# Kernel tuning notes

Hardware: AMD Instinct MI355X
Metric: run time of the kernel (lower is better)

## Reference

```python
import jax, jax.numpy as jnp
import numpy as np

SCORE_THRESHOLD = 0.5
IOU_THRESHOLD = 0.5


def _pairwise_iou(boxes):
    # boxes: [N, 4] in xyxy
    x1, y1, x2, y2 = boxes[:, 0], boxes[:, 1], boxes[:, 2], boxes[:, 3]
    area = (x2 - x1) * (y2 - y1)  # [N]
    ix1 = jnp.maximum(x1[:, None], x1[None, :])
    iy1 = jnp.maximum(y1[:, None], y1[None, :])
    ix2 = jnp.minimum(x2[:, None], x2[None, :])
    iy2 = jnp.minimum(y2[:, None], y2[None, :])
    iw = jnp.clip(ix2 - ix1, 0.0)
    ih = jnp.clip(iy2 - iy1, 0.0)
    inter = iw * ih  # [N, N]
    union = area[:, None] + area[None, :] - inter
    return inter / jnp.maximum(union, 1e-9)


def setup_inputs() -> dict:
    key = jax.random.key(0)
    rtdetr_raw_out = jax.random.uniform(key, (1, 8192, 5), dtype=jnp.float32)
    return {"rtdetr_raw_out": rtdetr_raw_out}


def reference(rtdetr_raw_out):
    x = rtdetr_raw_out[0]                      # [N, 5]
    cxcywh = x[:, :4]
    conf = x[:, 4]
    conf = conf / jnp.max(conf)                # normalize by max score
    cx, cy, w, h = cxcywh[:, 0], cxcywh[:, 1], cxcywh[:, 2], cxcywh[:, 3]
    xyxy = jnp.stack([cx - w * 0.5, cy - h * 0.5, cx + w * 0.5, cy + h * 0.5], axis=1)
    valid = conf >= SCORE_THRESHOLD            # score filter
    N = xyxy.shape[0]
    # sort by descending score (torchvision nms processes boxes in score order)
    order = jnp.argsort(-conf)
    boxes_s = xyxy[order]
    scores_s = conf[order]
    valid_s = valid[order]
    iou = _pairwise_iou(boxes_s)               # [N, N]
    idx = jnp.arange(N)

    def body(i, keep):
        # if box i survives, suppress all lower-score boxes with IoU > thr
        sup = keep[i] & (iou[i] > IOU_THRESHOLD) & (idx > i)
        return keep & ~sup

    keep = jax.lax.fori_loop(0, N, body, valid_s)
    out = jnp.concatenate([boxes_s, scores_s[:, None]], axis=1)  # [N, 5]
    # fixed-shape output: suppressed / below-threshold rows are zeroed
    return jnp.where(keep[:, None], out, 0.0)
```

## Files before the change

kernel.cpp:

```cpp
#include <hip/hip_runtime.h>
#include <cstdint>

typedef unsigned long long ull;

#define N_BOX 8192
#define N_WORDS 128
#define CH 512
#define WPC 8
#define NCH 16

#define OFF_TB     0
#define OFF_TD     3932160
#define OFF_BOXES  4456448
#define OFF_SCORES 4587520
#define OFF_RANK   4620288
#define OFF_MASK   4653056
#define OFF_MAXC   4654080
#define OFF_VB     4654084

__device__ __forceinline__ int rows_before(int c) {
    return 8192 * c - 256 * c * (c + 1);
}

__device__ __forceinline__ ull make_key(float s, int idx) {
    return (((ull)__float_as_uint(s)) << 13) | (ull)(8191 - idx);
}

__device__ __forceinline__ float box_area(float4 b) {
    return __fmul_rn(__fsub_rn(b.z, b.x), __fsub_rn(b.w, b.y));
}

__device__ __forceinline__ bool iou_gt_half(float4 a, float aarea, float4 b, float barea) {
    float ix1 = fmaxf(a.x, b.x);
    float iy1 = fmaxf(a.y, b.y);
    float ix2 = fminf(a.z, b.z);
    float iy2 = fminf(a.w, b.w);
    float iw = fmaxf(__fsub_rn(ix2, ix1), 0.0f);
    float ih = fmaxf(__fsub_rn(iy2, iy1), 0.0f);
    float inter = __fmul_rn(iw, ih);
    float uni = __fsub_rn(__fadd_rn(aarea, barea), inter);
    float iou = __fdiv_rn(inter, fmaxf(uni, 1e-9f));
    return iou > 0.5f;
}

__global__ __launch_bounds__(1024) void k1_max_zero(const float* __restrict__ in,
                                                    float* __restrict__ maxc,
                                                    int* __restrict__ rank,
                                                    ull* __restrict__ mask,
                                                    int* __restrict__ vbp) {
    int t = threadIdx.x;
    float m = 0.0f;
    for (int k = t; k < N_BOX; k += 1024) m = fmaxf(m, in[k * 5 + 4]);
    for (int off = 32; off; off >>= 1) m = fmaxf(m, __shfl_down(m, off));
    __shared__ float wm[16];
    if ((t & 63) == 0) wm[t >> 6] = m;
    __syncthreads();
    if (t == 0) {
        float mm = wm[0];
        for (int k = 1; k < 16; ++k) mm = fmaxf(mm, wm[k]);
        *maxc = mm;
        *vbp = 0;
    }
    for (int k = t; k < N_BOX; k += 1024) rank[k] = 0;
    if (t < N_WORDS) mask[t] = 0ull;
}

__global__ __launch_bounds__(256) void k2_rank(const float* __restrict__ in,
                                               const float* __restrict__ maxc_p,
                                               int* __restrict__ rank) {
    __shared__ ull keys[1024];
    int t = threadIdx.x;
    int bx = blockIdx.x;
    int it = bx & 31;
    int jt = bx >> 5;
    float maxc = *maxc_p;
    for (int r = 0; r < 4; ++r) {
        int j = jt * 1024 + r * 256 + t;
        float s = __fdiv_rn(in[j * 5 + 4], maxc);
        keys[r * 256 + t] = make_key(s, j);
    }
    __syncthreads();
    int i = it * 256 + t;
    ull ki = make_key(__fdiv_rn(in[i * 5 + 4], maxc), i);
    int cnt = 0;
    #pragma unroll 8
    for (int k = 0; k < 1024; ++k) cnt += (keys[k] > ki) ? 1 : 0;
    atomicAdd(&rank[i], cnt);
}

__global__ __launch_bounds__(256) void k3_scatter(const float* __restrict__ in,
                                                  const int* __restrict__ rank,
                                                  const float* __restrict__ maxc_p,
                                                  float4* __restrict__ boxes4,
                                                  float* __restrict__ scores,
                                                  ull* __restrict__ mask,
                                                  int* __restrict__ vbp) {
    int i = blockIdx.x * 256 + threadIdx.x;
    float cx = in[i * 5 + 0];
    float cy = in[i * 5 + 1];
    float w  = in[i * 5 + 2];
    float h  = in[i * 5 + 3];
    float c  = in[i * 5 + 4];
    float maxc = *maxc_p;
    float s = __fdiv_rn(c, maxc);
    int r = rank[i];
    float4 b;
    b.x = __fsub_rn(cx, __fmul_rn(w, 0.5f));
    b.y = __fsub_rn(cy, __fmul_rn(h, 0.5f));
    b.z = __fadd_rn(cx, __fmul_rn(w, 0.5f));
    b.w = __fadd_rn(cy, __fmul_rn(h, 0.5f));
    boxes4[r] = b;
    scores[r] = s;
    if (s >= 0.5f) {
        atomicOr(&mask[r >> 6], 1ull << (r & 63));
        atomicAdd(vbp, 1);
    }
}

__global__ __launch_bounds__(256) void k4_build(const float4* __restrict__ boxes4,
                                                const float* __restrict__ scores,
                                                ull* __restrict__ TB,
                                                ull* __restrict__ TD) {
    __shared__ float4 sb[CH];
    __shared__ float sa[CH];
    int bid = blockIdx.x;
    int t = threadIdx.x;
    int c, j0;
    bool diag;
    if (bid >= 1920) {
        diag = true;
        int d = bid - 1920;
        c = d >> 4;
        j0 = (d & 15) * 32;
    } else {
        diag = false;
        c = 0;
        int rem = bid;
        while (rem >= 240 - 16 * c) { rem -= 240 - 16 * c; ++c; }
        j0 = CH * (c + 1) + rem * 32;
    }
    if (scores[c * CH] < 0.5f) return;
    if (!diag && scores[j0] < 0.5f) return;

    for (int i = t; i < CH; i += 256) {
        float4 b = boxes4[c * CH + i];
        sb[i] = b;
        sa[i] = box_area(b);
    }
    __syncthreads();

    int w = t & 7;
    int jj = j0 + (t >> 3);
    if (diag) {
        int jl = jj;
        float4 me = sb[jl];
        float ma = sa[jl];
        int wj = jl >> 6;
        int lim = (w < wj) ? 64 : ((w == wj) ? (jl & 63) : 0);
        ull bits = 0;
        for (int k = 0; k < lim; ++k)
            if (iou_gt_half(sb[w * 64 + k], sa[w * 64 + k], me, ma)) bits |= 1ull << k;
        TD[c * 4096 + w * 512 + jl] = bits;
    } else {
        int j = jj;
        float4 me = boxes4[j];
        float ma = box_area(me);
        ull bits = 0;
        for (int k = 0; k < 64; ++k)
            if (iou_gt_half(sb[w * 64 + k], sa[w * 64 + k], me, ma)) bits |= 1ull << k;
        TB[(size_t)(rows_before(c) + (j - CH * (c + 1))) * WPC + w] = bits;
    }
}

__global__ __launch_bounds__(1024) void k5_nms(const float4* __restrict__ boxes4,
                                               const float* __restrict__ scores,
                                               const ull* __restrict__ gmask,
                                               const ull* __restrict__ TBg,
                                               const ull* __restrict__ TDg,
                                               const int* __restrict__ vbp,
                                               float* __restrict__ out) {
    __shared__ ull TDb[2][CH * WPC];
    __shared__ unsigned amask32[2 * N_WORDS];
    __shared__ ull keptw[WPC];
    __shared__ int svb;
    int t = threadIdx.x;
    int lane = t & 63;
    int wave = t >> 6;

    if (t < 2 * N_WORDS) amask32[t] = ((const unsigned*)gmask)[t];
    if (t == 0) svb = *vbp;
    if (t < WPC) keptw[t] = 0;
    for (int i = t; i < CH * WPC; i += 1024) TDb[0][i] = TDg[i];
    __syncthreads();

    int vb = svb;
    int nchv = (vb + CH - 1) / CH;
    int cur = 0;
    for (int c = 0; c < nchv; ++c) {
        if (wave == 0) {
            const ull* T = TDb[cur];
            ull alive[WPC];
            #pragma unroll
            for (int w = 0; w < WPC; ++w)
                alive[w] = (ull)amask32[c * 16 + 2 * w] |
                           ((ull)amask32[c * 16 + 2 * w + 1] << 32);
            #pragma unroll
            for (int w = 0; w < WPC; ++w) {
                ull word = alive[w];
                if (!word) continue;
                ull td = T[w * 512 + w * 64 + lane];
                ull a2 = word, kept = 0;
                while (a2 & ~kept) {
                    bool al = (a2 >> lane) & 1;
                    bool kp = (kept >> lane) & 1;
                    ull nk = __ballot(al && !kp && ((td & a2) == 0));
                    ull nd = __ballot(al && !kp && ((td & kept) != 0));
                    kept |= nk;
                    a2 &= ~nd;
                }
                alive[w] = kept;
                #pragma unroll
                for (int j = 0; j < WPC; ++j) {
                    if (j <= w) continue;
                    if (!alive[j]) continue;
                    ull m = T[w * 512 + j * 64 + lane];
                    alive[j] &= ~__ballot((m & kept) != 0);
                }
            }
            if (lane == 0) {
                #pragma unroll
                for (int w = 0; w < WPC; ++w) {
                    amask32[c * 16 + 2 * w]     = (unsigned)alive[w];
                    amask32[c * 16 + 2 * w + 1] = (unsigned)(alive[w] >> 32);
                    keptw[w] = alive[w];
                }
            }
        } else if (c + 1 < nchv) {
            int base = (c + 1) * CH * WPC;
            for (int i = t - 64; i < CH * WPC; i += 960) TDb[cur ^ 1][i] = TDg[base + i];
        }
        __syncthreads();

        ull kw[WPC];
        ull anyk = 0;
        #pragma unroll
        for (int k = 0; k < WPC; ++k) { kw[k] = keptw[k]; anyk |= kw[k]; }
        if (anyk) {
            const ull* TBc = TBg + (size_t)rows_before(c) * WPC;
            int jbase = CH * (c + 1);
            for (int j = jbase + t; j < vb; j += 1024) {
                if ((amask32[j >> 5] >> (j & 31)) & 1u) {
                    const ull* r = TBc + (size_t)(j - jbase) * WPC;
                    ull acc = 0;
                    #pragma unroll
                    for (int k = 0; k < WPC; ++k) acc |= r[k] & kw[k];
                    if (acc) atomicAnd(&amask32[j >> 5], ~(1u << (j & 31)));
                }
            }
        }
        cur ^= 1;
        __syncthreads();
    }

    #pragma unroll
    for (int rr = 0; rr < 8; ++rr) {
        int j = t * 8 + rr;
        bool kept = (amask32[j >> 5] >> (j & 31)) & 1u;
        float4 b = boxes4[j];
        float s = scores[j];
        out[j * 5 + 0] = kept ? b.x : 0.0f;
        out[j * 5 + 1] = kept ? b.y : 0.0f;
        out[j * 5 + 2] = kept ? b.z : 0.0f;
        out[j * 5 + 3] = kept ? b.w : 0.0f;
        out[j * 5 + 4] = kept ? s   : 0.0f;
    }
}

extern "C" void kernel_launch(void* const* d_in, const int* in_sizes, int n_in,
                              void* d_out, int out_size, void* d_ws, size_t ws_size,
                              hipStream_t stream) {
    const float* in = (const float*)d_in[0];
    char* ws = (char*)d_ws;
    ull* TB        = (ull*)(ws + OFF_TB);
    ull* TD        = (ull*)(ws + OFF_TD);
    float4* boxes4 = (float4*)(ws + OFF_BOXES);
    float* scores  = (float*)(ws + OFF_SCORES);
    int* rank      = (int*)(ws + OFF_RANK);
    ull* mask      = (ull*)(ws + OFF_MASK);
    float* maxc    = (float*)(ws + OFF_MAXC);
    int* vbp       = (int*)(ws + OFF_VB);
    float* out     = (float*)d_out;

    k1_max_zero<<<1, 1024, 0, stream>>>(in, maxc, rank, mask, vbp);
    k2_rank<<<256, 256, 0, stream>>>(in, maxc, rank);
    k3_scatter<<<32, 256, 0, stream>>>(in, rank, maxc, boxes4, scores, mask, vbp);
    k4_build<<<2176, 256, 0, stream>>>(boxes4, scores, TB, TD);
    k5_nms<<<1, 1024, 0, stream>>>(boxes4, scores, mask, TB, TD, vbp, out);
}
```

Before: 144.7 us.

## Fuse all NMS stages into one cooperative kernel with grid syncs

Replaces the five separate kernel launches (max, rank, scatter, IoU bitmask build, serial NMS) with a single cooperative kernel of 256 blocks of 1024 threads, separated by grid-wide barriers. The ranking now loads all 8192 keys into shared memory per block and does the counting within a block instead of using global atomics. The bitmask build is remapped onto 544 virtual tiles of 128 rows. This aims to remove per-launch overhead and the global rank zeroing. In exchange it pays for grid syncs, needs cooperative launch residency, and uses a 64KB shared union that may lower occupancy.

```diff
diff --git a/kernel.cpp b/kernel.cpp
--- a/kernel.cpp
+++ b/kernel.cpp
@@ -1,21 +1,22 @@
 #include <hip/hip_runtime.h>
+#include <hip/hip_cooperative_groups.h>
 #include <cstdint>
 
+namespace cg = cooperative_groups;
 typedef unsigned long long ull;
 
 #define N_BOX 8192
 #define N_WORDS 128
 #define CH 512
 #define WPC 8
-#define NCH 16
+#define NBLK 256
 
 #define OFF_TB     0
 #define OFF_TD     3932160
 #define OFF_BOXES  4456448
 #define OFF_SCORES 4587520
-#define OFF_RANK   4620288
+#define OFF_PART   4620288
 #define OFF_MASK   4653056
-#define OFF_MAXC   4654080
 #define OFF_VB     4654084
 
 __device__ __forceinline__ int rows_before(int c) {
@@ -43,154 +44,144 @@
     return iou > 0.5f;
 }
 
-__global__ __launch_bounds__(1024) void k1_max_zero(const float* __restrict__ in,
-                                                    float* __restrict__ maxc,
-                                                    int* __restrict__ rank,
-                                                    ull* __restrict__ mask,
-                                                    int* __restrict__ vbp) {
-    int t = threadIdx.x;
-    float m = 0.0f;
-    for (int k = t; k < N_BOX; k += 1024) m = fmaxf(m, in[k * 5 + 4]);
-    for (int off = 32; off; off >>= 1) m = fmaxf(m, __shfl_down(m, off));
-    __shared__ float wm[16];
-    if ((t & 63) == 0) wm[t >> 6] = m;
-    __syncthreads();
-    if (t == 0) {
-        float mm = wm[0];
-        for (int k = 1; k < 16; ++k) mm = fmaxf(mm, wm[k]);
-        *maxc = mm;
-        *vbp = 0;
-    }
-    for (int k = t; k < N_BOX; k += 1024) rank[k] = 0;
-    if (t < N_WORDS) mask[t] = 0ull;
-}
-
-__global__ __launch_bounds__(256) void k2_rank(const float* __restrict__ in,
-                                               const float* __restrict__ maxc_p,
-                                               int* __restrict__ rank) {
-    __shared__ ull keys[1024];
-    int t = threadIdx.x;
-    int bx = blockIdx.x;
-    int it = bx & 31;
-    int jt = bx >> 5;
-    float maxc = *maxc_p;
-    for (int r = 0; r < 4; ++r) {
-        int j = jt * 1024 + r * 256 + t;
-        float s = __fdiv_rn(in[j * 5 + 4], maxc);
-        keys[r * 256 + t] = make_key(s, j);
-    }
-    __syncthreads();
-    int i = it * 256 + t;
-    ull ki = make_key(__fdiv_rn(in[i * 5 + 4], maxc), i);
-    int cnt = 0;
-    #pragma unroll 8
-    for (int k = 0; k < 1024; ++k) cnt += (keys[k] > ki) ? 1 : 0;
-    atomicAdd(&rank[i], cnt);
-}
-
-__global__ __launch_bounds__(256) void k3_scatter(const float* __restrict__ in,
-                                                  const int* __restrict__ rank,
-                                                  const float* __restrict__ maxc_p,
-                                                  float4* __restrict__ boxes4,
-                                                  float* __restrict__ scores,
-                                                  ull* __restrict__ mask,
-                                                  int* __restrict__ vbp) {
-    int i = blockIdx.x * 256 + threadIdx.x;
-    float cx = in[i * 5 + 0];
-    float cy = in[i * 5 + 1];
-    float w  = in[i * 5 + 2];
-    float h  = in[i * 5 + 3];
-    float c  = in[i * 5 + 4];
-    float maxc = *maxc_p;
-    float s = __fdiv_rn(c, maxc);
-    int r = rank[i];
-    float4 b;
-    b.x = __fsub_rn(cx, __fmul_rn(w, 0.5f));
-    b.y = __fsub_rn(cy, __fmul_rn(h, 0.5f));
-    b.z = __fadd_rn(cx, __fmul_rn(w, 0.5f));
-    b.w = __fadd_rn(cy, __fmul_rn(h, 0.5f));
-    boxes4[r] = b;
-    scores[r] = s;
-    if (s >= 0.5f) {
-        atomicOr(&mask[r >> 6], 1ull << (r & 63));
-        atomicAdd(vbp, 1);
-    }
-}
-
-__global__ __launch_bounds__(256) void k4_build(const float4* __restrict__ boxes4,
-                                                const float* __restrict__ scores,
-                                                ull* __restrict__ TB,
-                                                ull* __restrict__ TD) {
-    __shared__ float4 sb[CH];
-    __shared__ float sa[CH];
-    int bid = blockIdx.x;
-    int t = threadIdx.x;
-    int c, j0;
-    bool diag;
-    if (bid >= 1920) {
-        diag = true;
-        int d = bid - 1920;
-        c = d >> 4;
-        j0 = (d & 15) * 32;
-    } else {
-        diag = false;
-        c = 0;
-        int rem = bid;
-        while (rem >= 240 - 16 * c) { rem -= 240 - 16 * c; ++c; }
-        j0 = CH * (c + 1) + rem * 32;
-    }
-    if (scores[c * CH] < 0.5f) return;
-    if (!diag && scores[j0] < 0.5f) return;
-
-    for (int i = t; i < CH; i += 256) {
-        float4 b = boxes4[c * CH + i];
-        sb[i] = b;
-        sa[i] = box_area(b);
-    }
-    __syncthreads();
-
-    int w = t & 7;
-    int jj = j0 + (t >> 3);
-    if (diag) {
-        int jl = jj;
-        float4 me = sb[jl];
-        float ma = sa[jl];
-        int wj = jl >> 6;
-        int lim = (w < wj) ? 64 : ((w == wj) ? (jl & 63) : 0);
-        ull bits = 0;
-        for (int k = 0; k < lim; ++k)
-            if (iou_gt_half(sb[w * 64 + k], sa[w * 64 + k], me, ma)) bits |= 1ull << k;
-        TD[c * 4096 + w * 512 + jl] = bits;
-    } else {
-        int j = jj;
-        float4 me = boxes4[j];
-        float ma = box_area(me);
-        ull bits = 0;
-        for (int k = 0; k < 64; ++k)
-            if (iou_gt_half(sb[w * 64 + k], sa[w * 64 + k], me, ma)) bits |= 1ull << k;
-        TB[(size_t)(rows_before(c) + (j - CH * (c + 1))) * WPC + w] = bits;
-    }
-}
-
-__global__ __launch_bounds__(1024) void k5_nms(const float4* __restrict__ boxes4,
-                                               const float* __restrict__ scores,
-                                               const ull* __restrict__ gmask,
-                                               const ull* __restrict__ TBg,
-                                               const ull* __restrict__ TDg,
-                                               const int* __restrict__ vbp,
-                                               float* __restrict__ out) {
-    __shared__ ull TDb[2][CH * WPC];
+struct SMemB { ull keys[N_BOX]; };
+struct SMemD { float4 sb[CH]; float sa[CH]; };
+struct SMemE { ull TDb[2][CH * WPC]; };
+union SMemU { SMemB b; SMemD d; SMemE e; };
+
+__global__ __launch_bounds__(1024, 4) void fused_nms(
+        const float* __restrict__ in,
+        ull* __restrict__ TB, ull* __restrict__ TD,
+        float4* __restrict__ boxes4, float* __restrict__ scores,
+        float* __restrict__ partials, ull* __restrict__ maskg,
+        int* __restrict__ vbp, float* __restrict__ out)
+{
+    __shared__ SMemU sm;
     __shared__ unsigned amask32[2 * N_WORDS];
     __shared__ ull keptw[WPC];
+    __shared__ float smax;
+    __shared__ int rnk[32];
     __shared__ int svb;
+    cg::grid_group grid = cg::this_grid();
+    int bid = blockIdx.x;
     int t = threadIdx.x;
     int lane = t & 63;
     int wave = t >> 6;
 
-    if (t < 2 * N_WORDS) amask32[t] = ((const unsigned*)gmask)[t];
+    if (t < 32) {
+        float c = in[(bid * 32 + t) * 5 + 4];
+        for (int off = 16; off; off >>= 1) c = fmaxf(c, __shfl_down(c, off));
+        if (t == 0) partials[bid] = c;
+    }
+    if (bid == 0) {
+        if (t < N_WORDS) maskg[t] = 0ull;
+        if (t == 0) *vbp = 0;
+    }
+    grid.sync();
+
+    if (t < 64) {
+        float m = fmaxf(fmaxf(partials[t], partials[t + 64]),
+                        fmaxf(partials[t + 128], partials[t + 192]));
+        for (int off = 32; off; off >>= 1) m = fmaxf(m, __shfl_down(m, off));
+        if (t == 0) smax = m;
+    }
+    if (t < 32) rnk[t] = 0;
+    __syncthreads();
+    float maxc = smax;
+    #pragma unroll
+    for (int r = 0; r < 8; ++r) {
+        int j = r * 1024 + t;
+        sm.b.keys[j] = make_key(__fdiv_rn(in[j * 5 + 4], maxc), j);
+    }
+    __syncthreads();
+    {
+        int i = bid * 32 + (t & 31);
+        ull ki = sm.b.keys[i];
+        int slice = t >> 5;
+        int cnt = 0;
+        #pragma unroll 8
+        for (int k = 0; k < 256; ++k) cnt += (sm.b.keys[slice * 256 + k] > ki) ? 1 : 0;
+        atomicAdd(&rnk[t & 31], cnt);
+    }
+    __syncthreads();
+
+    if (t < 32) {
+        int ii = bid * 32 + t;
+        float cx = in[ii * 5 + 0];
+        float cy = in[ii * 5 + 1];
+        float w  = in[ii * 5 + 2];
+        float h  = in[ii * 5 + 3];
+        float s  = __fdiv_rn(in[ii * 5 + 4], maxc);
+        int r = rnk[t];
+        float4 b;
+        b.x = __fsub_rn(cx, __fmul_rn(w, 0.5f));
+        b.y = __fsub_rn(cy, __fmul_rn(h, 0.5f));
+        b.z = __fadd_rn(cx, __fmul_rn(w, 0.5f));
+        b.w = __fadd_rn(cy, __fmul_rn(h, 0.5f));
+        boxes4[r] = b;
+        scores[r] = s;
+        if (s >= 0.5f) {
+            atomicOr(&maskg[r >> 6], 1ull << (r & 63));
+            atomicAdd(vbp, 1);
+        }
+    }
+    grid.sync();
+
+    for (int vt = bid; vt < 544; vt += NBLK) {
+        int c, jt;
+        bool diag;
+        if (vt < 64) { diag = true; c = vt >> 2; jt = vt & 3; }
+        else {
+            diag = false;
+            int id = vt - 64;
+            c = 0;
+            while (id >= 60 - 4 * c) { id -= 60 - 4 * c; ++c; }
+            jt = id;
+        }
+        bool active = (scores[c * CH] >= 0.5f);
+        int j0 = diag ? (jt * 128) : (CH * (c + 1) + jt * 128);
+        if (active && !diag) active = (scores[j0] >= 0.5f);
+        if (active) {
+            __syncthreads();
+            if (t < CH) {
+                float4 b = boxes4[c * CH + t];
+                sm.d.sb[t] = b;
+                sm.d.sa[t] = box_area(b);
+            }
+            __syncthreads();
+            int r = t >> 3;
+            int w = t & 7;
+            if (diag) {
+                int jl = j0 + r;
+                float4 me = sm.d.sb[jl];
+                float ma = sm.d.sa[jl];
+                int wj = jl >> 6;
+                int lim = (w < wj) ? 64 : ((w == wj) ? (jl & 63) : 0);
+                ull bits = 0;
+                for (int k = 0; k < lim; ++k)
+                    if (iou_gt_half(sm.d.sb[w * 64 + k], sm.d.sa[w * 64 + k], me, ma))
+                        bits |= 1ull << k;
+                TD[c * 4096 + w * 512 + jl] = bits;
+            } else {
+                int j = j0 + r;
+                float4 me = boxes4[j];
+                float ma = box_area(me);
+                ull bits = 0;
+                for (int k = 0; k < 64; ++k)
+                    if (iou_gt_half(sm.d.sb[w * 64 + k], sm.d.sa[w * 64 + k], me, ma))
+                        bits |= 1ull << k;
+                TB[(size_t)(rows_before(c) + (j - CH * (c + 1))) * WPC + w] = bits;
+            }
+        }
+    }
+    grid.sync();
+
+    if (bid != 0) return;
+
+    if (t < 2 * N_WORDS) amask32[t] = ((const unsigned*)maskg)[t];
     if (t == 0) svb = *vbp;
     if (t < WPC) keptw[t] = 0;
-    for (int i = t; i < CH * WPC; i += 1024) TDb[0][i] = TDg[i];
+    for (int i2 = t; i2 < CH * WPC; i2 += 1024) sm.e.TDb[0][i2] = TD[i2];
     __syncthreads();
 
     int vb = svb;
@@ -198,7 +189,7 @@
     int cur = 0;
     for (int c = 0; c < nchv; ++c) {
         if (wave == 0) {
-            const ull* T = TDb[cur];
+            const ull* T = sm.e.TDb[cur];
             ull alive[WPC];
             #pragma unroll
             for (int w = 0; w < WPC; ++w)
@@ -237,7 +228,8 @@
             }
         } else if (c + 1 < nchv) {
             int base = (c + 1) * CH * WPC;
-            for (int i = t - 64; i < CH * WPC; i += 960) TDb[cur ^ 1][i] = TDg[base + i];
+            for (int i2 = t - 64; i2 < CH * WPC; i2 += 960)
+                sm.e.TDb[cur ^ 1][i2] = TD[base + i2];
         }
         __syncthreads();
 
@@ -246,7 +238,7 @@
         #pragma unroll
         for (int k = 0; k < WPC; ++k) { kw[k] = keptw[k]; anyk |= kw[k]; }
         if (anyk) {
-            const ull* TBc = TBg + (size_t)rows_before(c) * WPC;
+            const ull* TBc = TB + (size_t)rows_before(c) * WPC;
             int jbase = CH * (c + 1);
             for (int j = jbase + t; j < vb; j += 1024) {
                 if ((amask32[j >> 5] >> (j & 31)) & 1u) {
@@ -285,15 +277,14 @@
     ull* TD        = (ull*)(ws + OFF_TD);
     float4* boxes4 = (float4*)(ws + OFF_BOXES);
     float* scores  = (float*)(ws + OFF_SCORES);
-    int* rank      = (int*)(ws + OFF_RANK);
-    ull* mask      = (ull*)(ws + OFF_MASK);
-    float* maxc    = (float*)(ws + OFF_MAXC);
+    float* partials= (float*)(ws + OFF_PART);
+    ull* maskg     = (ull*)(ws + OFF_MASK);
     int* vbp       = (int*)(ws + OFF_VB);
     float* out     = (float*)d_out;
 
-    k1_max_zero<<<1, 1024, 0, stream>>>(in, maxc, rank, mask, vbp);
-    k2_rank<<<256, 256, 0, stream>>>(in, maxc, rank);
-    k3_scatter<<<32, 256, 0, stream>>>(in, rank, maxc, boxes4, scores, mask, vbp);
-    k4_build<<<2176, 256, 0, stream>>>(boxes4, scores, TB, TD);
-    k5_nms<<<1, 1024, 0, stream>>>(boxes4, scores, mask, TB, TD, vbp, out);
-}
+    void* args[] = { (void*)&in, (void*)&TB, (void*)&TD, (void*)&boxes4,
+                     (void*)&scores, (void*)&partials, (void*)&maskg,
+                     (void*)&vbp, (void*)&out };
+    hipLaunchCooperativeKernel(reinterpret_cast<void*>(fused_nms),
+                               dim3(NBLK), dim3(1024), args, 0, stream);
+}
```

Result: slower. 213.0 us (+47.3%).

## Replace column suppression scan with per-kept-box row bitmask and ballot-based ranking

Applied to the files above, without the earlier changes.

The cross-chunk suppression matrix is now stored row-major per box (`sup[i][W]`, 80 words wide), so each kept box clears alive bits through atomic ANDs on its own row. Before, every candidate scanned a column. The rank kernel counts with wave ballots and popcount instead of per-thread comparison loops over shared memory. The max reduction is split across 32 blocks using an integer atomicMax. `SUPW` caps suppression at 5120 boxes, which assumes the valid count stays under that limit. The atomicMax also relies on `maxc` not holding a larger stale value from a previous call.

```diff
diff --git a/kernel.cpp b/kernel.cpp
--- a/kernel.cpp
+++ b/kernel.cpp
@@ -7,20 +7,16 @@
 #define N_WORDS 128
 #define CH 512
 #define WPC 8
-#define NCH 16
-
-#define OFF_TB     0
-#define OFF_TD     3932160
-#define OFF_BOXES  4456448
-#define OFF_SCORES 4587520
-#define OFF_RANK   4620288
-#define OFF_MASK   4653056
-#define OFF_MAXC   4654080
-#define OFF_VB     4654084
-
-__device__ __forceinline__ int rows_before(int c) {
-    return 8192 * c - 256 * c * (c + 1);
-}
+#define SUPW 80
+
+#define OFF_SUP    0
+#define OFF_TD     5242880
+#define OFF_BOXES  5767168
+#define OFF_SCORES 5898240
+#define OFF_RANK   5931008
+#define OFF_MASK   5963776
+#define OFF_MAXC   5964800
+#define OFF_VB     5964804
 
 __device__ __forceinline__ ull make_key(float s, int idx) {
     return (((ull)__float_as_uint(s)) << 13) | (ull)(8191 - idx);
@@ -43,49 +39,52 @@
     return iou > 0.5f;
 }
 
-__global__ __launch_bounds__(1024) void k1_max_zero(const float* __restrict__ in,
-                                                    float* __restrict__ maxc,
-                                                    int* __restrict__ rank,
-                                                    ull* __restrict__ mask,
-                                                    int* __restrict__ vbp) {
+__global__ __launch_bounds__(256) void k1_max_zero(const float* __restrict__ in,
+                                                   int* __restrict__ maxci,
+                                                   int* __restrict__ rank,
+                                                   ull* __restrict__ mask,
+                                                   int* __restrict__ vbp) {
     int t = threadIdx.x;
-    float m = 0.0f;
-    for (int k = t; k < N_BOX; k += 1024) m = fmaxf(m, in[k * 5 + 4]);
-    for (int off = 32; off; off >>= 1) m = fmaxf(m, __shfl_down(m, off));
-    __shared__ float wm[16];
-    if ((t & 63) == 0) wm[t >> 6] = m;
+    int i = blockIdx.x * 256 + t;
+    float c = in[i * 5 + 4];
+    for (int off = 32; off; off >>= 1) c = fmaxf(c, __shfl_down(c, off));
+    __shared__ float wm[4];
+    if ((t & 63) == 0) wm[t >> 6] = c;
     __syncthreads();
     if (t == 0) {
-        float mm = wm[0];
-        for (int k = 1; k < 16; ++k) mm = fmaxf(mm, wm[k]);
-        *maxc = mm;
-        *vbp = 0;
-    }
-    for (int k = t; k < N_BOX; k += 1024) rank[k] = 0;
-    if (t < N_WORDS) mask[t] = 0ull;
-}
-
-__global__ __launch_bounds__(256) void k2_rank(const float* __restrict__ in,
-                                               const float* __restrict__ maxc_p,
-                                               int* __restrict__ rank) {
-    __shared__ ull keys[1024];
+        float m = fmaxf(fmaxf(wm[0], wm[1]), fmaxf(wm[2], wm[3]));
+        atomicMax(maxci, __float_as_int(m));
+    }
+    rank[i] = 0;
+    if (blockIdx.x == 0) {
+        if (t < N_WORDS) mask[t] = 0ull;
+        if (t == 0) *vbp = 0;
+    }
+}
+
+__global__ __launch_bounds__(1024) void k2_rank(const float* __restrict__ in,
+                                                const float* __restrict__ maxc_p,
+                                                int* __restrict__ rank) {
     int t = threadIdx.x;
-    int bx = blockIdx.x;
-    int it = bx & 31;
-    int jt = bx >> 5;
+    int lane = t & 63;
+    int g = blockIdx.x * 16 + (t >> 6);
+    int jg = g & 127;
+    int ibase = (g >> 7) * 256;
     float maxc = *maxc_p;
-    for (int r = 0; r < 4; ++r) {
-        int j = jt * 1024 + r * 256 + t;
-        float s = __fdiv_rn(in[j * 5 + 4], maxc);
-        keys[r * 256 + t] = make_key(s, j);
-    }
-    __syncthreads();
-    int i = it * 256 + t;
-    ull ki = make_key(__fdiv_rn(in[i * 5 + 4], maxc), i);
-    int cnt = 0;
-    #pragma unroll 8
-    for (int k = 0; k < 1024; ++k) cnt += (keys[k] > ki) ? 1 : 0;
-    atomicAdd(&rank[i], cnt);
+    int j = jg * 64 + lane;
+    ull kj = make_key(__fdiv_rn(in[j * 5 + 4], maxc), j);
+    #pragma unroll 1
+    for (int blk = 0; blk < 4; ++blk) {
+        int cnt = 0;
+        #pragma unroll 8
+        for (int ii = 0; ii < 64; ++ii) {
+            int i = ibase + blk * 64 + ii;
+            ull ki = make_key(__fdiv_rn(in[i * 5 + 4], maxc), i);
+            int pc = __popcll(__ballot(kj > ki));
+            cnt = (lane == ii) ? pc : cnt;
+        }
+        atomicAdd(&rank[ibase + blk * 64 + lane], cnt);
+    }
 }
 
 __global__ __launch_bounds__(256) void k3_scatter(const float* __restrict__ in,
@@ -119,63 +118,70 @@
 
 __global__ __launch_bounds__(256) void k4_build(const float4* __restrict__ boxes4,
                                                 const float* __restrict__ scores,
-                                                ull* __restrict__ TB,
+                                                ull* __restrict__ sup,
                                                 ull* __restrict__ TD) {
-    __shared__ float4 sb[CH];
-    __shared__ float sa[CH];
     int bid = blockIdx.x;
     int t = threadIdx.x;
-    int c, j0;
-    bool diag;
-    if (bid >= 1920) {
-        diag = true;
-        int d = bid - 1920;
-        c = d >> 4;
-        j0 = (d & 15) * 32;
+    if (bid < 4096) {
+        int it = bid >> 5;
+        int wt = bid & 31;
+        int i0 = it * 64;
+        if (wt * 4 >= SUPW) return;
+        if ((wt + 1) * 256 <= i0) return;
+        if (scores[i0] < 0.5f) return;
+        if (scores[wt * 256] < 0.5f) return;
+        __shared__ float4 bi[64];
+        __shared__ float4 bj[256];
+        if (t < 64) bi[t] = boxes4[i0 + t];
+        bj[t] = boxes4[wt * 256 + t];
+        __syncthreads();
+        int il = t >> 2;
+        int wl = t & 3;
+        int i = i0 + il;
+        float4 a = bi[il];
+        float aarea = box_area(a);
+        ull word = 0ull;
+        #pragma unroll 4
+        for (int k = 0; k < 64; ++k) {
+            float4 b = bj[wl * 64 + k];
+            if (iou_gt_half(a, aarea, b, box_area(b))) word |= (1ull << k);
+        }
+        sup[(size_t)i * SUPW + wt * 4 + wl] = word;
     } else {
-        diag = false;
-        c = 0;
-        int rem = bid;
-        while (rem >= 240 - 16 * c) { rem -= 240 - 16 * c; ++c; }
-        j0 = CH * (c + 1) + rem * 32;
-    }
-    if (scores[c * CH] < 0.5f) return;
-    if (!diag && scores[j0] < 0.5f) return;
-
-    for (int i = t; i < CH; i += 256) {
-        float4 b = boxes4[c * CH + i];
-        sb[i] = b;
-        sa[i] = box_area(b);
-    }
-    __syncthreads();
-
-    int w = t & 7;
-    int jj = j0 + (t >> 3);
-    if (diag) {
-        int jl = jj;
+        int d = bid - 4096;
+        int c = d >> 3;
+        int jt = d & 7;
+        if (scores[c * CH] < 0.5f) return;
+        __shared__ float4 sb[CH];
+        __shared__ float sa[CH];
+        for (int i2 = t; i2 < CH; i2 += 256) {
+            float4 b = boxes4[c * CH + i2];
+            sb[i2] = b;
+            sa[i2] = box_area(b);
+        }
+        __syncthreads();
+        int r = t >> 2;
+        int wl = t & 3;
+        int jl = jt * 64 + r;
         float4 me = sb[jl];
         float ma = sa[jl];
         int wj = jl >> 6;
-        int lim = (w < wj) ? 64 : ((w == wj) ? (jl & 63) : 0);
-        ull bits = 0;
-        for (int k = 0; k < lim; ++k)
-            if (iou_gt_half(sb[w * 64 + k], sa[w * 64 + k], me, ma)) bits |= 1ull << k;
-        TD[c * 4096 + w * 512 + jl] = bits;
-    } else {
-        int j = jj;
-        float4 me = boxes4[j];
-        float ma = box_area(me);
-        ull bits = 0;
-        for (int k = 0; k < 64; ++k)
-            if (iou_gt_half(sb[w * 64 + k], sa[w * 64 + k], me, ma)) bits |= 1ull << k;
-        TB[(size_t)(rows_before(c) + (j - CH * (c + 1))) * WPC + w] = bits;
+        #pragma unroll
+        for (int p = 0; p < 2; ++p) {
+            int w = wl + p * 4;
+            int lim = (w < wj) ? 64 : ((w == wj) ? (jl & 63) : 0);
+            ull bits = 0;
+            for (int k = 0; k < lim; ++k)
+                if (iou_gt_half(sb[w * 64 + k], sa[w * 64 + k], me, ma)) bits |= 1ull << k;
+            TD[c * 4096 + w * 512 + jl] = bits;
+        }
     }
 }
 
 __global__ __launch_bounds__(1024) void k5_nms(const float4* __restrict__ boxes4,
                                                const float* __restrict__ scores,
                                                const ull* __restrict__ gmask,
-                                               const ull* __restrict__ TBg,
+                                               const ull* __restrict__ supg,
                                                const ull* __restrict__ TDg,
                                                const int* __restrict__ vbp,
                                                float* __restrict__ out) {
@@ -190,11 +196,13 @@
     if (t < 2 * N_WORDS) amask32[t] = ((const unsigned*)gmask)[t];
     if (t == 0) svb = *vbp;
     if (t < WPC) keptw[t] = 0;
-    for (int i = t; i < CH * WPC; i += 1024) TDb[0][i] = TDg[i];
+    for (int i2 = t; i2 < CH * WPC; i2 += 1024) TDb[0][i2] = TDg[i2];
     __syncthreads();
 
     int vb = svb;
     int nchv = (vb + CH - 1) / CH;
+    int wv = (vb + 63) >> 6;
+    int Wlim = (wv < SUPW) ? wv : SUPW;
     int cur = 0;
     for (int c = 0; c < nchv; ++c) {
         if (wave == 0) {
@@ -207,7 +215,7 @@
             #pragma unroll
             for (int w = 0; w < WPC; ++w) {
                 ull word = alive[w];
-                if (!word) continue;
+                if (!word) { if (lane == 0) keptw[w] = 0; continue; }
                 ull td = T[w * 512 + w * 64 + lane];
                 ull a2 = word, kept = 0;
                 while (a2 & ~kept) {
@@ -226,36 +234,44 @@
                     ull m = T[w * 512 + j * 64 + lane];
                     alive[j] &= ~__ballot((m & kept) != 0);
                 }
+                if (lane == 0) keptw[w] = kept;
             }
             if (lane == 0) {
                 #pragma unroll
                 for (int w = 0; w < WPC; ++w) {
                     amask32[c * 16 + 2 * w]     = (unsigned)alive[w];
                     amask32[c * 16 + 2 * w + 1] = (unsigned)(alive[w] >> 32);
-                    keptw[w] = alive[w];
                 }
             }
         } else if (c + 1 < nchv) {
             int base = (c + 1) * CH * WPC;
-            for (int i = t - 64; i < CH * WPC; i += 960) TDb[cur ^ 1][i] = TDg[base + i];
+            for (int i2 = t - 64; i2 < CH * WPC; i2 += 960)
+                TDb[cur ^ 1][i2] = TDg[base + i2];
         }
         __syncthreads();
 
-        ull kw[WPC];
-        ull anyk = 0;
-        #pragma unroll
-        for (int k = 0; k < WPC; ++k) { kw[k] = keptw[k]; anyk |= kw[k]; }
-        if (anyk) {
-            const ull* TBc = TBg + (size_t)rows_before(c) * WPC;
-            int jbase = CH * (c + 1);
-            for (int j = jbase + t; j < vb; j += 1024) {
-                if ((amask32[j >> 5] >> (j & 31)) & 1u) {
-                    const ull* r = TBc + (size_t)(j - jbase) * WPC;
-                    ull acc = 0;
-                    #pragma unroll
-                    for (int k = 0; k < WPC; ++k) acc |= r[k] & kw[k];
-                    if (acc) atomicAnd(&amask32[j >> 5], ~(1u << (j & 31)));
+        int kidx = 0;
+        for (int w8 = 0; w8 < WPC; ++w8) {
+            ull kw = keptw[w8];
+            while (kw) {
+                int b = __builtin_ctzll(kw);
+                kw &= kw - 1;
+                if ((kidx & 15) == wave) {
+                    int i = c * CH + w8 * 64 + b;
+                    const ull* row = supg + (size_t)i * SUPW;
+                    for (int Wb = WPC * (c + 1); Wb < Wlim; Wb += 64) {
+                        int W = Wb + lane;
+                        if (W < Wlim) {
+                            ull s = row[W];
+                            if (s) {
+                                unsigned lo = (unsigned)s, hi = (unsigned)(s >> 32);
+                                if (lo) atomicAnd(&amask32[2 * W], ~lo);
+                                if (hi) atomicAnd(&amask32[2 * W + 1], ~hi);
+                            }
+                        }
+                    }
                 }
+                ++kidx;
             }
         }
         cur ^= 1;
@@ -281,7 +297,7 @@
                               hipStream_t stream) {
     const float* in = (const float*)d_in[0];
     char* ws = (char*)d_ws;
-    ull* TB        = (ull*)(ws + OFF_TB);
+    ull* sup       = (ull*)(ws + OFF_SUP);
     ull* TD        = (ull*)(ws + OFF_TD);
     float4* boxes4 = (float4*)(ws + OFF_BOXES);
     float* scores  = (float*)(ws + OFF_SCORES);
@@ -291,9 +307,9 @@
     int* vbp       = (int*)(ws + OFF_VB);
     float* out     = (float*)d_out;
 
-    k1_max_zero<<<1, 1024, 0, stream>>>(in, maxc, rank, mask, vbp);
-    k2_rank<<<256, 256, 0, stream>>>(in, maxc, rank);
+    k1_max_zero<<<32, 256, 0, stream>>>(in, (int*)maxc, rank, mask, vbp);
+    k2_rank<<<256, 1024, 0, stream>>>(in, maxc, rank);
     k3_scatter<<<32, 256, 0, stream>>>(in, rank, maxc, boxes4, scores, mask, vbp);
-    k4_build<<<2176, 256, 0, stream>>>(boxes4, scores, TB, TD);
-    k5_nms<<<1, 1024, 0, stream>>>(boxes4, scores, mask, TB, TD, vbp, out);
-}
+    k4_build<<<4224, 256, 0, stream>>>(boxes4, scores, sup, TD);
+    k5_nms<<<1, 1024, 0, stream>>>(boxes4, scores, mask, sup, TD, vbp, out);
+}
```

New measurement: 274.9 us. +90.1%, slower.

## Fuse max, rank and scatter kernels; derive valid mask from sorted prefix count

Applied to the files above, without the earlier changes.

Merges the max-reduction, rank-counting and scatter kernels into one kernel. Each of 32 blocks recomputes the global max and builds all 8192 sort keys in shared memory, then counts ranks for its own 256 boxes. The NMS kernel now counts valid scores itself and builds the alive mask as a prefix, since sorted valid boxes are contiguous. This removes the per-row mask test in the suppression loop. The aim is to cut two kernel launches plus the global atomics and zeroing, at the cost of redundant max and key work in every block.

```diff
diff --git a/kernel.cpp b/kernel.cpp
--- a/kernel.cpp
+++ b/kernel.cpp
@@ -7,16 +7,11 @@
 #define N_WORDS 128
 #define CH 512
 #define WPC 8
-#define NCH 16
 
 #define OFF_TB     0
 #define OFF_TD     3932160
 #define OFF_BOXES  4456448
 #define OFF_SCORES 4587520
-#define OFF_RANK   4620288
-#define OFF_MASK   4653056
-#define OFF_MAXC   4654080
-#define OFF_VB     4654084
 
 __device__ __forceinline__ int rows_before(int c) {
     return 8192 * c - 256 * c * (c + 1);
@@ -43,81 +38,69 @@
     return iou > 0.5f;
 }
 
-__global__ __launch_bounds__(1024) void k1_max_zero(const float* __restrict__ in,
-                                                    float* __restrict__ maxc,
-                                                    int* __restrict__ rank,
-                                                    ull* __restrict__ mask,
-                                                    int* __restrict__ vbp) {
+__global__ __launch_bounds__(1024) void ka_rank_scatter(const float* __restrict__ in,
+                                                        float4* __restrict__ boxes4,
+                                                        float* __restrict__ scores) {
+    __shared__ ull skeys[N_BOX];
+    __shared__ float wm[16];
+    __shared__ int rnk[256];
     int t = threadIdx.x;
+    int bid = blockIdx.x;
+
+    float cf[8];
     float m = 0.0f;
-    for (int k = t; k < N_BOX; k += 1024) m = fmaxf(m, in[k * 5 + 4]);
+    #pragma unroll
+    for (int k = 0; k < 8; ++k) {
+        cf[k] = in[(k * 1024 + t) * 5 + 4];
+        m = fmaxf(m, cf[k]);
+    }
     for (int off = 32; off; off >>= 1) m = fmaxf(m, __shfl_down(m, off));
-    __shared__ float wm[16];
     if ((t & 63) == 0) wm[t >> 6] = m;
-    __syncthreads();
-    if (t == 0) {
-        float mm = wm[0];
-        for (int k = 1; k < 16; ++k) mm = fmaxf(mm, wm[k]);
-        *maxc = mm;
-        *vbp = 0;
-    }
-    for (int k = t; k < N_BOX; k += 1024) rank[k] = 0;
-    if (t < N_WORDS) mask[t] = 0ull;
-}
-
-__global__ __launch_bounds__(256) void k2_rank(const float* __restrict__ in,
-                                               const float* __restrict__ maxc_p,
-                                               int* __restrict__ rank) {
-    __shared__ ull keys[1024];
-    int t = threadIdx.x;
-    int bx = blockIdx.x;
-    int it = bx & 31;
-    int jt = bx >> 5;
-    float maxc = *maxc_p;
-    for (int r = 0; r < 4; ++r) {
-        int j = jt * 1024 + r * 256 + t;
-        float s = __fdiv_rn(in[j * 5 + 4], maxc);
-        keys[r * 256 + t] = make_key(s, j);
-    }
-    __syncthreads();
-    int i = it * 256 + t;
-    ull ki = make_key(__fdiv_rn(in[i * 5 + 4], maxc), i);
-    int cnt = 0;
-    #pragma unroll 8
-    for (int k = 0; k < 1024; ++k) cnt += (keys[k] > ki) ? 1 : 0;
-    atomicAdd(&rank[i], cnt);
-}
-
-__global__ __launch_bounds__(256) void k3_scatter(const float* __restrict__ in,
-                                                  const int* __restrict__ rank,
-                                                  const float* __restrict__ maxc_p,
-                                                  float4* __restrict__ boxes4,
-                                                  float* __restrict__ scores,
-                                                  ull* __restrict__ mask,
-                                                  int* __restrict__ vbp) {
-    int i = blockIdx.x * 256 + threadIdx.x;
-    float cx = in[i * 5 + 0];
-    float cy = in[i * 5 + 1];
-    float w  = in[i * 5 + 2];
-    float h  = in[i * 5 + 3];
-    float c  = in[i * 5 + 4];
-    float maxc = *maxc_p;
-    float s = __fdiv_rn(c, maxc);
-    int r = rank[i];
-    float4 b;
-    b.x = __fsub_rn(cx, __fmul_rn(w, 0.5f));
-    b.y = __fsub_rn(cy, __fmul_rn(h, 0.5f));
-    b.z = __fadd_rn(cx, __fmul_rn(w, 0.5f));
-    b.w = __fadd_rn(cy, __fmul_rn(h, 0.5f));
-    boxes4[r] = b;
-    scores[r] = s;
-    if (s >= 0.5f) {
-        atomicOr(&mask[r >> 6], 1ull << (r & 63));
-        atomicAdd(vbp, 1);
-    }
-}
-
-__global__ __launch_bounds__(256) void k4_build(const float4* __restrict__ boxes4,
+    if (t < 256) rnk[t] = 0;
+    __syncthreads();
+    float maxc = wm[0];
+    #pragma unroll
+    for (int k = 1; k < 16; ++k) maxc = fmaxf(maxc, wm[k]);
+
+    #pragma unroll
+    for (int k = 0; k < 8; ++k) {
+        int j = k * 1024 + t;
+        skeys[j] = make_key(__fdiv_rn(cf[k], maxc), j);
+    }
+    __syncthreads();
+
+    {
+        int il = t & 255;
+        int i = bid * 256 + il;
+        ull ki = skeys[i];
+        int q = t >> 8;
+        int cnt = 0;
+        #pragma unroll 8
+        for (int k = q * 2048; k < (q + 1) * 2048; ++k)
+            cnt += (skeys[k] > ki) ? 1 : 0;
+        atomicAdd(&rnk[il], cnt);
+    }
+    __syncthreads();
+
+    if (t < 256) {
+        int i = bid * 256 + t;
+        float cx = in[i * 5 + 0];
+        float cy = in[i * 5 + 1];
+        float w  = in[i * 5 + 2];
+        float h  = in[i * 5 + 3];
+        float s  = __fdiv_rn(in[i * 5 + 4], maxc);
+        int r = rnk[t];
+        float4 b;
+        b.x = __fsub_rn(cx, __fmul_rn(w, 0.5f));
+        b.y = __fsub_rn(cy, __fmul_rn(h, 0.5f));
+        b.z = __fadd_rn(cx, __fmul_rn(w, 0.5f));
+        b.w = __fadd_rn(cy, __fmul_rn(h, 0.5f));
+        boxes4[r] = b;
+        scores[r] = s;
+    }
+}
+
+__global__ __launch_bounds__(256) void kb_build(const float4* __restrict__ boxes4,
                                                 const float* __restrict__ scores,
                                                 ull* __restrict__ TB,
                                                 ull* __restrict__ TD) {
@@ -172,12 +155,10 @@
     }
 }
 
-__global__ __launch_bounds__(1024) void k5_nms(const float4* __restrict__ boxes4,
+__global__ __launch_bounds__(1024) void kc_nms(const float4* __restrict__ boxes4,
                                                const float* __restrict__ scores,
-                                               const ull* __restrict__ gmask,
                                                const ull* __restrict__ TBg,
                                                const ull* __restrict__ TDg,
-                                               const int* __restrict__ vbp,
                                                float* __restrict__ out) {
     __shared__ ull TDb[2][CH * WPC];
     __shared__ unsigned amask32[2 * N_WORDS];
@@ -187,13 +168,29 @@
     int lane = t & 63;
     int wave = t >> 6;
 
-    if (t < 2 * N_WORDS) amask32[t] = ((const unsigned*)gmask)[t];
-    if (t == 0) svb = *vbp;
+    if (t == 0) svb = 0;
+    __syncthreads();
+    {
+        int cnt = 0;
+        #pragma unroll
+        for (int k = 0; k < 8; ++k) cnt += (scores[k * 1024 + t] >= 0.5f) ? 1 : 0;
+        ull bal = __ballot(cnt > 0);
+        (void)bal;
+        for (int off = 32; off; off >>= 1) cnt += __shfl_down(cnt, off);
+        if (lane == 0) atomicAdd(&svb, cnt);
+    }
+    __syncthreads();
+    int vb = svb;
+
+    if (t < 2 * N_WORDS) {
+        int base = (t >> 1) * 64 + (t & 1) * 32;
+        int n = vb - base;
+        amask32[t] = (n >= 32) ? 0xffffffffu : ((n <= 0) ? 0u : ((1u << n) - 1u));
+    }
     if (t < WPC) keptw[t] = 0;
-    for (int i = t; i < CH * WPC; i += 1024) TDb[0][i] = TDg[i];
-    __syncthreads();
-
-    int vb = svb;
+    for (int i2 = t; i2 < CH * WPC; i2 += 1024) TDb[0][i2] = TDg[i2];
+    __syncthreads();
+
     int nchv = (vb + CH - 1) / CH;
     int cur = 0;
     for (int c = 0; c < nchv; ++c) {
@@ -237,7 +234,8 @@
             }
         } else if (c + 1 < nchv) {
             int base = (c + 1) * CH * WPC;
-            for (int i = t - 64; i < CH * WPC; i += 960) TDb[cur ^ 1][i] = TDg[base + i];
+            for (int i2 = t - 64; i2 < CH * WPC; i2 += 960)
+                TDb[cur ^ 1][i2] = TDg[base + i2];
         }
         __syncthreads();
 
@@ -249,13 +247,11 @@
             const ull* TBc = TBg + (size_t)rows_before(c) * WPC;
             int jbase = CH * (c + 1);
             for (int j = jbase + t; j < vb; j += 1024) {
-                if ((amask32[j >> 5] >> (j & 31)) & 1u) {
-                    const ull* r = TBc + (size_t)(j - jbase) * WPC;
-                    ull acc = 0;
-                    #pragma unroll
-                    for (int k = 0; k < WPC; ++k) acc |= r[k] & kw[k];
-                    if (acc) atomicAnd(&amask32[j >> 5], ~(1u << (j & 31)));
-                }
+                const ull* r = TBc + (size_t)(j - jbase) * WPC;
+                ull acc = 0;
+                #pragma unroll
+                for (int k = 0; k < WPC; ++k) acc |= r[k] & kw[k];
+                if (acc) atomicAnd(&amask32[j >> 5], ~(1u << (j & 31)));
             }
         }
         cur ^= 1;
@@ -285,15 +281,9 @@
     ull* TD        = (ull*)(ws + OFF_TD);
     float4* boxes4 = (float4*)(ws + OFF_BOXES);
     float* scores  = (float*)(ws + OFF_SCORES);
-    int* rank      = (int*)(ws + OFF_RANK);
-    ull* mask      = (ull*)(ws + OFF_MASK);
-    float* maxc    = (float*)(ws + OFF_MAXC);
-    int* vbp       = (int*)(ws + OFF_VB);
     float* out     = (float*)d_out;
 
-    k1_max_zero<<<1, 1024, 0, stream>>>(in, maxc, rank, mask, vbp);
-    k2_rank<<<256, 256, 0, stream>>>(in, maxc, rank);
-    k3_scatter<<<32, 256, 0, stream>>>(in, rank, maxc, boxes4, scores, mask, vbp);
-    k4_build<<<2176, 256, 0, stream>>>(boxes4, scores, TB, TD);
-    k5_nms<<<1, 1024, 0, stream>>>(boxes4, scores, mask, TB, TD, vbp, out);
-}
+    ka_rank_scatter<<<32, 1024, 0, stream>>>(in, boxes4, scores);
+    kb_build<<<2176, 256, 0, stream>>>(boxes4, scores, TB, TD);
+    kc_nms<<<1, 1024, 0, stream>>>(boxes4, scores, TB, TD, out);
+}
```

Measured after the change: 166.6 us. 15.2% more time.
